# Kernel tuning notes

Measured on AMD Instinct MI355X. Metric: run time of the kernel, lower is better.

The kernel has to match this reference:

```python
import jax, jax.numpy as jnp
import numpy as np

N_NODES = 100000
N_EDGES = 1000000
D_FEAT = 64
N_GRAPHS = 64


def setup_inputs() -> dict:
    key = jax.random.key(0)
    ks = jax.random.split(key, 5)
    x = jax.random.normal(ks[0], (N_NODES, D_FEAT), dtype=jnp.float32)
    edge_index = jax.random.randint(ks[1], (2, N_EDGES), 0, N_NODES, dtype=jnp.int32)
    batch = jnp.sort(jax.random.randint(ks[2], (N_NODES,), 0, N_GRAPHS, dtype=jnp.int32))
    s = 1.0 / np.sqrt(D_FEAT)
    W1 = jax.random.uniform(ks[3], (D_FEAT, D_FEAT), jnp.float32, -s, s)
    W2 = jax.random.uniform(ks[4], (D_FEAT, D_FEAT), jnp.float32, -s, s)
    b1 = jnp.zeros((D_FEAT,), jnp.float32)
    b2 = jnp.zeros((D_FEAT,), jnp.float32)
    return {"x": x, "edge_index": edge_index, "batch": batch,
            "W1": W1, "b1": b1, "W2": W2, "b2": b2}


def gcn_conv(x, edge_index, W, b, num_nodes):
    # PyG GCNConv: h = D^{-1/2} (A + I) D^{-1/2} (x W) + b
    loops = jnp.arange(num_nodes, dtype=edge_index.dtype)
    row = jnp.concatenate([edge_index[0], loops])  # source nodes
    col = jnp.concatenate([edge_index[1], loops])  # target nodes
    h = x @ W  # [N, D]
    deg = jax.ops.segment_sum(jnp.ones_like(col, dtype=h.dtype), col,
                              num_segments=num_nodes)  # >= 1 due to self loops
    dinv = jax.lax.rsqrt(deg)
    norm = dinv[row] * dinv[col]  # [E+N]
    out = jax.ops.segment_sum(h[row] * norm[:, None], col, num_segments=num_nodes)
    return out + b


def reference(x, edge_index, batch, W1, b1, W2, b2):
    n = x.shape[0]
    h = gcn_conv(x, edge_index, W1, b1, n)
    h = gcn_conv(h, edge_index, W2, b2, n)
    # global_mean_pool over graph ids
    sums = jax.ops.segment_sum(h, batch, num_segments=N_GRAPHS)  # [G, D]
    cnts = jax.ops.segment_sum(jnp.ones((n, 1), h.dtype), batch,
                               num_segments=N_GRAPHS)
    return sums / jnp.maximum(cnts, 1.0)
```

## Files before the change

### kernel.cpp

```cpp
#include <hip/hip_runtime.h>
#include <hip/hip_fp16.h>

#define DFEAT 64
#define NG 64
#define TILE 128
#define NBLK 256
#define NBMAX 1024

__global__ __launch_bounds__(256) void k_cnt(const int* __restrict__ col,
                                             int* __restrict__ cnt_m,
                                             int e, int nb, int chunk) {
  __shared__ int hist[NBMAX];
  int tid = threadIdx.x;
  int blk = blockIdx.x;
  for (int b = tid; b < nb; b += 256) hist[b] = 0;
  __syncthreads();
  int lo = blk * chunk, hi = min(lo + chunk, e);
  for (int i = lo + tid; i < hi; i += 256)
    atomicAdd(&hist[col[i] >> 7], 1);
  __syncthreads();
  for (int b = tid; b < nb; b += 256)
    cnt_m[(size_t)blk * nb + b] = hist[b];
}

__global__ __launch_bounds__(256) void k_colscan(int* __restrict__ cnt_m,
                                                 int* __restrict__ gcount, int nb) {
  __shared__ int sh[256];
  int tid = threadIdx.x;
  int b = blockIdx.x;
  int v = cnt_m[(size_t)tid * nb + b];
  sh[tid] = v;
  __syncthreads();
  for (int off = 1; off < 256; off <<= 1) {
    int t = (tid >= off) ? sh[tid - off] : 0;
    __syncthreads();
    sh[tid] += t;
    __syncthreads();
  }
  cnt_m[(size_t)tid * nb + b] = sh[tid] - v;
  if (tid == 255) gcount[b] = sh[255];
}

__global__ __launch_bounds__(1024) void k_bscan(const int* __restrict__ gcount,
                                                int* __restrict__ base, int nb) {
  __shared__ int sh[1024];
  int tid = threadIdx.x;
  int v = (tid < nb) ? gcount[tid] : 0;
  sh[tid] = v;
  __syncthreads();
  for (int off = 1; off < 1024; off <<= 1) {
    int t = (tid >= off) ? sh[tid - off] : 0;
    __syncthreads();
    sh[tid] += t;
    __syncthreads();
  }
  if (tid < nb) base[tid] = sh[tid] - v;
  if (tid == 0) base[nb] = sh[1023];
}

__global__ __launch_bounds__(256) void k_bin2(const int* __restrict__ row,
                                              const int* __restrict__ col,
                                              const int* __restrict__ base,
                                              const int* __restrict__ cnt_m,
                                              int* __restrict__ pairs,
                                              int e, int nb, int chunk) {
  __shared__ int gl[NBMAX];
  __shared__ int lcur[NBMAX];
  int tid = threadIdx.x;
  int blk = blockIdx.x;
  for (int b = tid; b < nb; b += 256) {
    gl[b] = base[b] + cnt_m[(size_t)blk * nb + b];
    lcur[b] = 0;
  }
  __syncthreads();
  int lo = blk * chunk, hi = min(lo + chunk, e);
  for (int i = lo + tid; i < hi; i += 256) {
    int s = row[i], t = col[i];
    int b = t >> 7;
    int pos = gl[b] + atomicAdd(&lcur[b], 1);
    pairs[pos] = s | ((t & (TILE - 1)) << 20);
  }
}

__global__ __launch_bounds__(256) void k_csr(const int* __restrict__ pairs,
                                             const int* __restrict__ base,
                                             int* __restrict__ starts,
                                             int* __restrict__ srcs,
                                             float* __restrict__ dinv,
                                             int n, int e) {
  __shared__ int cnt[TILE];
  __shared__ int cur[TILE];
  __shared__ int sc[TILE];
  int tid = threadIdx.x;
  int b = blockIdx.x;
  int tile0 = b * TILE;
  if (tid < TILE) cnt[tid] = 0;
  __syncthreads();
  int e0 = base[b], e1 = base[b + 1];
  for (int i = e0 + tid; i < e1; i += 256)
    atomicAdd(&cnt[(unsigned)pairs[i] >> 20], 1);
  __syncthreads();
  int c = (tid < TILE) ? cnt[tid] : 0;
  if (tid < TILE) sc[tid] = c;
  __syncthreads();
  for (int off = 1; off < TILE; off <<= 1) {
    int t = (tid < TILE && tid >= off) ? sc[tid - off] : 0;
    __syncthreads();
    if (tid < TILE) sc[tid] += t;
    __syncthreads();
  }
  if (tid < TILE) {
    int excl = sc[tid] - c;
    cur[tid] = excl;
    int node = tile0 + tid;
    if (node < n) {
      starts[node] = e0 + excl;
      dinv[node] = rsqrtf(1.0f + (float)c);
    }
  }
  if (b == 0 && tid == 0) starts[n] = e;
  __syncthreads();
  for (int i = e0 + tid; i < e1; i += 256) {
    int p = pairs[i];
    int pos = atomicAdd(&cur[(unsigned)p >> 20], 1);
    srcs[e0 + pos] = p & 0xFFFFF;
  }
}

__global__ void k_half(const float* __restrict__ x, __half2* __restrict__ xh,
                       int n32) {
  int i = blockIdx.x * 256 + threadIdx.x;
  if (i < n32) {
    float2 v = ((const float2*)x)[i];
    xh[i] = __float22half2_rn(v);
  }
}

__global__ __launch_bounds__(256) void k_w12(const float* __restrict__ W1,
                                             const float* __restrict__ W2,
                                             const float* __restrict__ b1,
                                             float* __restrict__ WW,
                                             float* __restrict__ bw) {
  __shared__ float w1[4096], w2[4096];
  int tid = threadIdx.x;
  for (int i = tid; i < 4096; i += 256) { w1[i] = W1[i]; w2[i] = W2[i]; }
  __syncthreads();
  for (int p = tid; p < 4096; p += 256) {
    int k = p >> 6, d = p & 63;
    float a = 0.f;
    for (int m = 0; m < 64; ++m) a += w1[k * 64 + m] * w2[m * 64 + d];
    WW[p] = a;
  }
  if (tid < 64) {
    float a = 0.f;
    for (int k = 0; k < 64; ++k) a += b1[k] * w2[k * 64 + tid];
    bw[tid] = a;
  }
}

__global__ __launch_bounds__(256) void k_gather1(const int* __restrict__ starts,
                                                 const int* __restrict__ srcs,
                                                 const float* __restrict__ dinv,
                                                 const __half2* __restrict__ xh,
                                                 __half2* __restrict__ z1h,
                                                 float* __restrict__ u, int n) {
  int node = blockIdx.x * 8 + (threadIdx.x >> 5);
  if (node >= n) return;
  int lh = threadIdx.x & 31;
  int s = starts[node];
  int deg = starts[node + 1] - s;
  float dc = dinv[node];
  float2 hs = __half22float2(xh[(size_t)node * 32 + lh]);
  float ax = 0.f, ay = 0.f, wsum = 0.f;
  int j = 0;
  for (; j + 3 < deg; j += 4) {
    int r0 = srcs[s + j + 0];
    int r1 = srcs[s + j + 1];
    int r2 = srcs[s + j + 2];
    int r3 = srcs[s + j + 3];
    float w0 = dinv[r0], w1 = dinv[r1], w2 = dinv[r2], w3 = dinv[r3];
    float2 v0 = __half22float2(xh[(size_t)r0 * 32 + lh]);
    float2 v1 = __half22float2(xh[(size_t)r1 * 32 + lh]);
    float2 v2 = __half22float2(xh[(size_t)r2 * 32 + lh]);
    float2 v3 = __half22float2(xh[(size_t)r3 * 32 + lh]);
    ax += w0 * v0.x + w1 * v1.x + w2 * v2.x + w3 * v3.x;
    ay += w0 * v0.y + w1 * v1.y + w2 * v2.y + w3 * v3.y;
    wsum += w0 + w1 + w2 + w3;
  }
  for (; j < deg; ++j) {
    int r = srcs[s + j];
    float w = dinv[r];
    float2 v = __half22float2(xh[(size_t)r * 32 + lh]);
    ax += w * v.x;
    ay += w * v.y;
    wsum += w;
  }
  float2 res;
  res.x = dc * dc * hs.x + dc * ax;
  res.y = dc * dc * hs.y + dc * ay;
  z1h[(size_t)node * 32 + lh] = __float22half2_rn(res);
  if (lh == 0) u[node] = dc * (dc + wsum);
}

__global__ __launch_bounds__(256) void k_gather2(const int* __restrict__ starts,
                                                 const int* __restrict__ srcs,
                                                 const float* __restrict__ dinv,
                                                 const __half2* __restrict__ z1h,
                                                 float* __restrict__ z2, int n) {
  int node = blockIdx.x * 8 + (threadIdx.x >> 5);
  if (node >= n) return;
  int lh = threadIdx.x & 31;
  int s = starts[node];
  int deg = starts[node + 1] - s;
  float dc = dinv[node];
  float2 hs = __half22float2(z1h[(size_t)node * 32 + lh]);
  float ax = 0.f, ay = 0.f;
  int j = 0;
  for (; j + 3 < deg; j += 4) {
    int r0 = srcs[s + j + 0];
    int r1 = srcs[s + j + 1];
    int r2 = srcs[s + j + 2];
    int r3 = srcs[s + j + 3];
    float w0 = dinv[r0], w1 = dinv[r1], w2 = dinv[r2], w3 = dinv[r3];
    float2 v0 = __half22float2(z1h[(size_t)r0 * 32 + lh]);
    float2 v1 = __half22float2(z1h[(size_t)r1 * 32 + lh]);
    float2 v2 = __half22float2(z1h[(size_t)r2 * 32 + lh]);
    float2 v3 = __half22float2(z1h[(size_t)r3 * 32 + lh]);
    ax += w0 * v0.x + w1 * v1.x + w2 * v2.x + w3 * v3.x;
    ay += w0 * v0.y + w1 * v1.y + w2 * v2.y + w3 * v3.y;
  }
  for (; j < deg; ++j) {
    int r = srcs[s + j];
    float w = dinv[r];
    float2 v = __half22float2(z1h[(size_t)r * 32 + lh]);
    ax += w * v.x;
    ay += w * v.y;
  }
  float2 res;
  res.x = dc * dc * hs.x + dc * ax;
  res.y = dc * dc * hs.y + dc * ay;
  *(float2*)(&z2[(size_t)node * 64 + lh * 2]) = res;
}

__global__ void k_pool2(const float* __restrict__ z2, const float* __restrict__ u,
                        const int* __restrict__ batch, float* __restrict__ S,
                        float* __restrict__ T, float* __restrict__ cntf, int n) {
  int d = threadIdx.x;
  int start = blockIdx.x * 64;
  if (start >= n) return;
  int end = min(start + 64, n);
  int curg = batch[start];
  float acc = 0.f, cnt = 0.f, ua = 0.f;
  for (int i = start; i < end; ++i) {
    int g = batch[i];
    if (g != curg) {
      unsafeAtomicAdd(&S[curg * 64 + d], acc);
      if (d == 0) {
        unsafeAtomicAdd(&cntf[curg], cnt);
        unsafeAtomicAdd(&T[curg], ua);
      }
      acc = 0.f; cnt = 0.f; ua = 0.f;
      curg = g;
    }
    acc += z2[(size_t)i * 64 + d];
    if (d == 0) { cnt += 1.f; ua += u[i]; }
  }
  unsafeAtomicAdd(&S[curg * 64 + d], acc);
  if (d == 0) {
    unsafeAtomicAdd(&cntf[curg], cnt);
    unsafeAtomicAdd(&T[curg], ua);
  }
}

__global__ __launch_bounds__(256) void k_final2(const float* __restrict__ S,
                                                const float* __restrict__ T,
                                                const float* __restrict__ cntf,
                                                const float* __restrict__ WW,
                                                const float* __restrict__ bw,
                                                const float* __restrict__ b2,
                                                float* __restrict__ out) {
  __shared__ float sS[4096], sW[4096];
  int tid = threadIdx.x;
  for (int i = tid; i < 4096; i += 256) { sS[i] = S[i]; sW[i] = WW[i]; }
  __syncthreads();
  for (int p = tid; p < 4096; p += 256) {
    int g = p >> 6, d = p & 63;
    float a = 0.f;
    for (int k = 0; k < 64; ++k) a += sS[g * 64 + k] * sW[k * 64 + d];
    float c = fmaxf(cntf[g], 1.0f);
    out[p] = (a + T[g] * bw[d]) / c + b2[d];
  }
}

extern "C" void kernel_launch(void* const* d_in, const int* in_sizes, int n_in,
                              void* d_out, int out_size, void* d_ws, size_t ws_size,
                              hipStream_t stream) {
  const float* x = (const float*)d_in[0];
  const int* ei = (const int*)d_in[1];
  const int* bat = (const int*)d_in[2];
  const float* W1 = (const float*)d_in[3];
  const float* b1 = (const float*)d_in[4];
  const float* W2 = (const float*)d_in[5];
  const float* b2 = (const float*)d_in[6];
  float* out = (float*)d_out;

  int n = in_sizes[0] / 64;
  int e = in_sizes[1] / 2;
  const int* rowp = ei;
  const int* colp = ei + e;
  int nb = (n + TILE - 1) / TILE;
  int chunk = (e + NBLK - 1) / NBLK;

  char* ws = (char*)d_ws;
  size_t off = 0;
  auto alloc = [&](size_t elems) {
    void* p = ws + off;
    off += ((elems * 4 + 255) & ~(size_t)255);
    return p;
  };
  float* S = (float*)alloc(NG * DFEAT);
  float* cntf = (float*)alloc(NG);
  float* T = (float*)alloc(NG);
  size_t zbytes = off;
  int* gcount = (int*)alloc(nb);
  int* base = (int*)alloc(nb + 1);
  int* cnt_m = (int*)alloc((size_t)NBLK * nb);
  float* dinv = (float*)alloc(n);
  int* starts = (int*)alloc(n + 1);
  int* srcs = (int*)alloc(e);
  float* u = (float*)alloc(n);
  float* WW = (float*)alloc(DFEAT * DFEAT);
  float* bw = (float*)alloc(DFEAT);
  __half2* xh = (__half2*)alloc((size_t)n * 32);
  __half2* z1h = (__half2*)alloc((size_t)n * 32);
  float* z2 = (float*)alloc((size_t)n * 64);
  int* pairs = (int*)z2;

  int nbw = (n + 7) / 8;
  int n32 = n * 32;

  hipMemsetAsync(S, 0, zbytes, stream);
  k_cnt<<<NBLK, 256, 0, stream>>>(colp, cnt_m, e, nb, chunk);
  k_colscan<<<nb, 256, 0, stream>>>(cnt_m, gcount, nb);
  k_bscan<<<1, 1024, 0, stream>>>(gcount, base, nb);
  k_bin2<<<NBLK, 256, 0, stream>>>(rowp, colp, base, cnt_m, pairs, e, nb, chunk);
  k_csr<<<nb, 256, 0, stream>>>(pairs, base, starts, srcs, dinv, n, e);
  k_half<<<(n32 + 255) / 256, 256, 0, stream>>>(x, xh, n32);
  k_w12<<<1, 256, 0, stream>>>(W1, W2, b1, WW, bw);

  k_gather1<<<nbw, 256, 0, stream>>>(starts, srcs, dinv, xh, z1h, u, n);
  k_gather2<<<nbw, 256, 0, stream>>>(starts, srcs, dinv, z1h, z2, n);

  k_pool2<<<(n + 63) / 64, 64, 0, stream>>>(z2, u, bat, S, T, cntf, n);
  k_final2<<<1, 256, 0, stream>>>(S, T, cntf, WW, bw, b2, out);
}
```

Measured before the change: 230.4 us.

## Prescale features by dinv and gather with 16-byte loads per 8-lane group

The half-precision copy of x is now multiplied by dinv for each source node as it is written. This lets the first gather drop its per-edge dinv weighting, and the stored z1 becomes dinv²-scaled so the second gather drops it too. Both gathers now give each node 8 lanes with float4 (16-byte) loads instead of 32 lanes with 4-byte loads, so fewer, wider memory transactions and more nodes per block. The trade-off is one extra dinv read in the conversion kernel, extra fp16 rounding of the scaled values, and more registers per lane.

```diff
diff --git a/kernel.cpp b/kernel.cpp
--- a/kernel.cpp
+++ b/kernel.cpp
@@ -127,12 +127,14 @@
   }
 }
 
-__global__ void k_half(const float* __restrict__ x, __half2* __restrict__ xh,
-                       int n32) {
+__global__ __launch_bounds__(256) void k_xs(const float* __restrict__ x,
+                                            const float* __restrict__ dinv,
+                                            __half2* __restrict__ xh, int n32) {
   int i = blockIdx.x * 256 + threadIdx.x;
   if (i < n32) {
     float2 v = ((const float2*)x)[i];
-    xh[i] = __float22half2_rn(v);
+    float d = dinv[i >> 5];
+    xh[i] = __floats2half2_rn(v.x * d, v.y * d);
   }
 }
 
@@ -158,48 +160,64 @@
   }
 }
 
+__device__ __forceinline__ void acc8(float2& a0, float2& a1, float2& a2,
+                                     float2& a3, float4 v) {
+  const __half2* hp = (const __half2*)&v;
+  float2 t;
+  t = __half22float2(hp[0]); a0.x += t.x; a0.y += t.y;
+  t = __half22float2(hp[1]); a1.x += t.x; a1.y += t.y;
+  t = __half22float2(hp[2]); a2.x += t.x; a2.y += t.y;
+  t = __half22float2(hp[3]); a3.x += t.x; a3.y += t.y;
+}
+
 __global__ __launch_bounds__(256) void k_gather1(const int* __restrict__ starts,
                                                  const int* __restrict__ srcs,
                                                  const float* __restrict__ dinv,
                                                  const __half2* __restrict__ xh,
                                                  __half2* __restrict__ z1h,
                                                  float* __restrict__ u, int n) {
-  int node = blockIdx.x * 8 + (threadIdx.x >> 5);
+  int node = blockIdx.x * 32 + (threadIdx.x >> 3);
   if (node >= n) return;
-  int lh = threadIdx.x & 31;
+  int l = threadIdx.x & 7;
   int s = starts[node];
   int deg = starts[node + 1] - s;
   float dc = dinv[node];
-  float2 hs = __half22float2(xh[(size_t)node * 32 + lh]);
-  float ax = 0.f, ay = 0.f, wsum = 0.f;
+  const float4* xf = (const float4*)xh;
+  float4 sv = xf[(size_t)node * 8 + l];
+  float2 a0 = make_float2(0.f, 0.f), a1 = a0, a2 = a0, a3 = a0;
+  acc8(a0, a1, a2, a3, sv);
+  float wsum = 0.f;
   int j = 0;
   for (; j + 3 < deg; j += 4) {
     int r0 = srcs[s + j + 0];
     int r1 = srcs[s + j + 1];
     int r2 = srcs[s + j + 2];
     int r3 = srcs[s + j + 3];
-    float w0 = dinv[r0], w1 = dinv[r1], w2 = dinv[r2], w3 = dinv[r3];
-    float2 v0 = __half22float2(xh[(size_t)r0 * 32 + lh]);
-    float2 v1 = __half22float2(xh[(size_t)r1 * 32 + lh]);
-    float2 v2 = __half22float2(xh[(size_t)r2 * 32 + lh]);
-    float2 v3 = __half22float2(xh[(size_t)r3 * 32 + lh]);
-    ax += w0 * v0.x + w1 * v1.x + w2 * v2.x + w3 * v3.x;
-    ay += w0 * v0.y + w1 * v1.y + w2 * v2.y + w3 * v3.y;
-    wsum += w0 + w1 + w2 + w3;
+    float4 v0 = xf[(size_t)r0 * 8 + l];
+    float4 v1 = xf[(size_t)r1 * 8 + l];
+    float4 v2 = xf[(size_t)r2 * 8 + l];
+    float4 v3 = xf[(size_t)r3 * 8 + l];
+    wsum += dinv[r0] + dinv[r1] + dinv[r2] + dinv[r3];
+    acc8(a0, a1, a2, a3, v0);
+    acc8(a0, a1, a2, a3, v1);
+    acc8(a0, a1, a2, a3, v2);
+    acc8(a0, a1, a2, a3, v3);
   }
   for (; j < deg; ++j) {
     int r = srcs[s + j];
-    float w = dinv[r];
-    float2 v = __half22float2(xh[(size_t)r * 32 + lh]);
-    ax += w * v.x;
-    ay += w * v.y;
-    wsum += w;
-  }
-  float2 res;
-  res.x = dc * dc * hs.x + dc * ax;
-  res.y = dc * dc * hs.y + dc * ay;
-  z1h[(size_t)node * 32 + lh] = __float22half2_rn(res);
-  if (lh == 0) u[node] = dc * (dc + wsum);
+    float4 v = xf[(size_t)r * 8 + l];
+    wsum += dinv[r];
+    acc8(a0, a1, a2, a3, v);
+  }
+  float s2 = dc * dc;
+  float4 ov;
+  __half2* op = (__half2*)&ov;
+  op[0] = __floats2half2_rn(s2 * a0.x, s2 * a0.y);
+  op[1] = __floats2half2_rn(s2 * a1.x, s2 * a1.y);
+  op[2] = __floats2half2_rn(s2 * a2.x, s2 * a2.y);
+  op[3] = __floats2half2_rn(s2 * a3.x, s2 * a3.y);
+  ((float4*)z1h)[(size_t)node * 8 + l] = ov;
+  if (l == 0) u[node] = dc * (dc + wsum);
 }
 
 __global__ __launch_bounds__(256) void k_gather2(const int* __restrict__ starts,
@@ -207,39 +225,39 @@
                                                  const float* __restrict__ dinv,
                                                  const __half2* __restrict__ z1h,
                                                  float* __restrict__ z2, int n) {
-  int node = blockIdx.x * 8 + (threadIdx.x >> 5);
+  int node = blockIdx.x * 32 + (threadIdx.x >> 3);
   if (node >= n) return;
-  int lh = threadIdx.x & 31;
+  int l = threadIdx.x & 7;
   int s = starts[node];
   int deg = starts[node + 1] - s;
   float dc = dinv[node];
-  float2 hs = __half22float2(z1h[(size_t)node * 32 + lh]);
-  float ax = 0.f, ay = 0.f;
+  const float4* xf = (const float4*)z1h;
+  float4 sv = xf[(size_t)node * 8 + l];
+  float2 a0 = make_float2(0.f, 0.f), a1 = a0, a2 = a0, a3 = a0;
+  acc8(a0, a1, a2, a3, sv);
   int j = 0;
   for (; j + 3 < deg; j += 4) {
     int r0 = srcs[s + j + 0];
     int r1 = srcs[s + j + 1];
     int r2 = srcs[s + j + 2];
     int r3 = srcs[s + j + 3];
-    float w0 = dinv[r0], w1 = dinv[r1], w2 = dinv[r2], w3 = dinv[r3];
-    float2 v0 = __half22float2(z1h[(size_t)r0 * 32 + lh]);
-    float2 v1 = __half22float2(z1h[(size_t)r1 * 32 + lh]);
-    float2 v2 = __half22float2(z1h[(size_t)r2 * 32 + lh]);
-    float2 v3 = __half22float2(z1h[(size_t)r3 * 32 + lh]);
-    ax += w0 * v0.x + w1 * v1.x + w2 * v2.x + w3 * v3.x;
-    ay += w0 * v0.y + w1 * v1.y + w2 * v2.y + w3 * v3.y;
+    float4 v0 = xf[(size_t)r0 * 8 + l];
+    float4 v1 = xf[(size_t)r1 * 8 + l];
+    float4 v2 = xf[(size_t)r2 * 8 + l];
+    float4 v3 = xf[(size_t)r3 * 8 + l];
+    acc8(a0, a1, a2, a3, v0);
+    acc8(a0, a1, a2, a3, v1);
+    acc8(a0, a1, a2, a3, v2);
+    acc8(a0, a1, a2, a3, v3);
   }
   for (; j < deg; ++j) {
     int r = srcs[s + j];
-    float w = dinv[r];
-    float2 v = __half22float2(z1h[(size_t)r * 32 + lh]);
-    ax += w * v.x;
-    ay += w * v.y;
-  }
-  float2 res;
-  res.x = dc * dc * hs.x + dc * ax;
-  res.y = dc * dc * hs.y + dc * ay;
-  *(float2*)(&z2[(size_t)node * 64 + lh * 2]) = res;
+    float4 v = xf[(size_t)r * 8 + l];
+    acc8(a0, a1, a2, a3, v);
+  }
+  float4* zr = (float4*)(z2 + (size_t)node * 64);
+  zr[l * 2 + 0] = make_float4(dc * a0.x, dc * a0.y, dc * a1.x, dc * a1.y);
+  zr[l * 2 + 1] = make_float4(dc * a2.x, dc * a2.y, dc * a3.x, dc * a3.y);
 }
 
 __global__ void k_pool2(const float* __restrict__ z2, const float* __restrict__ u,
@@ -336,7 +354,7 @@
   float* z2 = (float*)alloc((size_t)n * 64);
   int* pairs = (int*)z2;
 
-  int nbw = (n + 7) / 8;
+  int nbw = (n + 31) / 32;
   int n32 = n * 32;
 
   hipMemsetAsync(S, 0, zbytes, stream);
@@ -345,7 +363,7 @@
   k_bscan<<<1, 1024, 0, stream>>>(gcount, base, nb);
   k_bin2<<<NBLK, 256, 0, stream>>>(rowp, colp, base, cnt_m, pairs, e, nb, chunk);
   k_csr<<<nb, 256, 0, stream>>>(pairs, base, starts, srcs, dinv, n, e);
-  k_half<<<(n32 + 255) / 256, 256, 0, stream>>>(x, xh, n32);
+  k_xs<<<(n32 + 255) / 256, 256, 0, stream>>>(x, dinv, xh, n32);
   k_w12<<<1, 256, 0, stream>>>(W1, W2, b1, WW, bw);
 
   k_gather1<<<nbw, 256, 0, stream>>>(starts, srcs, dinv, xh, z1h, u, n);
```

Result: faster. 214.3 us (-7.0%).
